# Kernel tuning notes

Measured on AMD Instinct MI355X. Metric: run time of the kernel, lower is better.

The kernel has to match this reference:

```python
import jax, jax.numpy as jnp
import numpy as np


def setup_inputs() -> dict:
    key = jax.random.key(0)
    ks = jax.random.split(key, 8)
    B, T, D = 4, 4096, 1024
    d_inner, dt_rank, d_state = 2048, 64, 16
    s = 0.02  # weight init scale for numerical stability
    f32 = jnp.float32
    return {
        "x": jax.random.normal(ks[0], (B, T, D), f32),
        "in_proj_w": jax.random.normal(ks[1], (2 * d_inner, D), f32) * s,
        "conv_w": jax.random.normal(ks[2], (d_inner, 1, 3), f32) * s,
        "conv_b": jnp.zeros((d_inner,), f32),
        "x_proj_w": jax.random.normal(ks[3], (dt_rank + 2 * d_state, d_inner), f32) * s,
        "dt_proj_w": jax.random.normal(ks[4], (d_inner, dt_rank), f32) * s,
        "dt_proj_b": jnp.zeros((d_inner,), f32),
        "D_param": jnp.ones((d_inner,), f32),
        "out_proj_w": jax.random.normal(ks[5], (D, d_inner), f32) * s,
    }


def reference(x, in_proj_w, conv_w, conv_b, x_proj_w, dt_proj_w, dt_proj_b, D_param, out_proj_w):
    d_inner = conv_b.shape[0]
    dt_rank = dt_proj_w.shape[1]

    # in_proj and split into x-branch / gate-branch z
    xz = jnp.einsum('btd,ed->bte', x, in_proj_w)          # [B,T,2*d_inner]
    xs, z = jnp.split(xz, 2, axis=-1)                     # each [B,T,d_inner]

    # depthwise conv1d along time (kernel 3, padding 1, groups=d_inner)
    xc = jnp.transpose(xs, (0, 2, 1))                     # [B,C,T]
    xc = jax.lax.conv_general_dilated(
        xc, conv_w, window_strides=(1,), padding=[(1, 1)],
        dimension_numbers=('NCH', 'OIH', 'NCH'), feature_group_count=d_inner)
    xc = xc + conv_b[None, :, None]
    xs = jnp.transpose(xc, (0, 2, 1))                     # [B,T,d_inner]

    # x_proj -> take dt part (B,C slices are unused by the scan math)
    x_dbl = jnp.einsum('btc,ec->bte', xs, x_proj_w)       # [B,T,dt_rank+2*d_state]
    dt = jnp.einsum('btr,cr->btc', x_dbl[..., :dt_rank], dt_proj_w) + dt_proj_b  # [B,T,d_inner]

    # selective scan: scalar gate per (batch, t); h_t = g*h_{t-1} + (1-g)*x_t
    gate = jax.nn.sigmoid(jnp.mean(dt, axis=-1))          # [B,T]

    def step(h, inp):
        g, xt = inp                                       # g: [B], xt: [B,d_inner]
        h_new = g[:, None] * h + (1.0 - g[:, None]) * xt
        return h_new, h_new

    h0 = jnp.zeros_like(xs[:, 0])                         # [B,d_inner]
    _, ys = jax.lax.scan(step, h0, (gate.T, jnp.transpose(xs, (1, 0, 2))))
    y = jnp.transpose(ys, (1, 0, 2))                      # [B,T,d_inner]

    y = y * jax.nn.silu(z) + D_param * xs
    return jnp.einsum('btc,dc->btd', y, out_proj_w)       # [B,T,d_model]
```

## Files before the change

### kernel.cpp

```cpp
#include <hip/hip_runtime.h>
#include <hip/hip_bf16.h>
#include <math.h>

#define B_ 4
#define T_ 4096
#define DM 1024
#define DI 2048
#define E2 4096
#define NCHUNK 128
#define CLEN 32

typedef __attribute__((ext_vector_type(8))) short short8;
typedef __attribute__((ext_vector_type(4))) float floatx4;

union bfs { __hip_bfloat16 b; short s; };

__device__ __forceinline__ float bf2f(__hip_bfloat16 x) { return __bfloat162float(x); }
__device__ __forceinline__ short f2s(float x) { bfs u; u.b = __float2bfloat16(x); return u.s; }

__device__ __forceinline__ float ldw(const void* p, int i, int f32m) {
    return f32m ? ((const float*)p)[i] : bf2f(((const __hip_bfloat16*)p)[i]);
}

#define GLDS16(gp, lp) __builtin_amdgcn_global_load_lds( \
    (const __attribute__((address_space(1))) void*)(gp), \
    (__attribute__((address_space(3))) void*)(lp), 16, 0, 0)

#define MEMFENCE asm volatile("" ::: "memory")

__global__ __launch_bounds__(256)
void detect_k(const unsigned short* __restrict__ xu, unsigned* __restrict__ flag)
{
    __shared__ int red[256];
    const int tid = threadIdx.x;
    int cnt = 0;
    for (int i = tid; i < 2048; i += 256) {
        const int e = (xu[i] >> 7) & 0xFF;
        cnt += (e >= 0x90);
    }
    red[tid] = cnt;
    __syncthreads();
    for (int off = 128; off; off >>= 1) {
        if (tid < off) red[tid] += red[tid + off];
        __syncthreads();
    }
    if (tid == 0) *flag = (red[0] >= 8) ? 1u : 0u;
}

__global__ __launch_bounds__(256)
void cvt_k(const void* __restrict__ src, __hip_bfloat16* __restrict__ dst,
           const unsigned* __restrict__ flag)
{
    const int fm = (int)*flag;
    const size_t i0 = ((size_t)blockIdx.x * 256 + threadIdx.x) * 8;
    if (fm) {
        const float* f = (const float*)src + i0;
        floatx4 lo = *(const floatx4*)f;
        floatx4 hi = *(const floatx4*)(f + 4);
        short8 r;
        r[0] = f2s(lo[0]); r[1] = f2s(lo[1]); r[2] = f2s(lo[2]); r[3] = f2s(lo[3]);
        r[4] = f2s(hi[0]); r[5] = f2s(hi[1]); r[6] = f2s(hi[2]); r[7] = f2s(hi[3]);
        *(short8*)(dst + i0) = r;
    } else {
        *(short8*)(dst + i0) = *(const short8*)((const __hip_bfloat16*)src + i0);
    }
}

__global__ __launch_bounds__(256)
void cvt_strided_k(const void* __restrict__ src, __hip_bfloat16* __restrict__ dst,
                   const unsigned* __restrict__ flag)
{
    const int fm = (int)*flag;
    const size_t i0 = ((size_t)blockIdx.x * 256 + threadIdx.x) * 8;
    const size_t row = i0 >> 11, col = i0 & 2047;
    __hip_bfloat16* d = dst + row * E2 + col;
    if (fm) {
        const float* f = (const float*)src + i0;
        floatx4 lo = *(const floatx4*)f;
        floatx4 hi = *(const floatx4*)(f + 4);
        short8 r;
        r[0] = f2s(lo[0]); r[1] = f2s(lo[1]); r[2] = f2s(lo[2]); r[3] = f2s(lo[3]);
        r[4] = f2s(hi[0]); r[5] = f2s(hi[1]); r[6] = f2s(hi[2]); r[7] = f2s(hi[3]);
        *(short8*)d = r;
    } else {
        *(short8*)d = *(const short8*)((const __hip_bfloat16*)src + i0);
    }
}

__global__ __launch_bounds__(512)
void gemm256(const __hip_bfloat16* __restrict__ A,
             const __hip_bfloat16* __restrict__ Bt,
             void* __restrict__ C, int K, int lda, int ldb, int ldc,
             int csel, const unsigned* __restrict__ flag)
{
    __shared__ __align__(16) char sL[4 * 32768];

    const int cf = csel & (int)*flag;

    const int tid  = threadIdx.x;
    const int lane = tid & 63;
    const int wid  = tid >> 6;
    const int wr   = wid >> 2;
    const int wc   = wid & 3;
    const int l15  = lane & 15;
    const int quad = lane >> 4;
    const int swl  = (l15 >> 1) & 3;

    const int m0 = blockIdx.x * 256;
    const int n0 = blockIdx.y * 256;

    floatx4 acc[8][4];
#pragma unroll
    for (int i = 0; i < 8; i++)
#pragma unroll
        for (int j = 0; j < 4; j++) acc[i][j] = (floatx4){0.f, 0.f, 0.f, 0.f};

    const int srow = tid >> 2;
    const int ksrc = (((tid & 3) ^ ((tid >> 3) & 3))) * 8;
    const __hip_bfloat16* gA = A  + (size_t)(m0 + srow) * lda + ksrc;
    const __hip_bfloat16* gB = Bt + (size_t)(n0 + srow) * ldb + ksrc;
    const size_t h1A = (size_t)128 * lda;
    const size_t h1B = (size_t)128 * ldb;

    char* const ldsW = sL + wid * 1024;

    const int NT = K >> 5;

#define STAGE_A(buf, kt) do { \
    const __hip_bfloat16* g_ = gA + (size_t)(kt) * 32; \
    char* l_ = ldsW + (buf) * 32768; \
    GLDS16(g_, l_); \
    GLDS16(g_ + h1A, l_ + 8192); } while (0)
#define STAGE_B(buf, kt) do { \
    const __hip_bfloat16* g_ = gB + (size_t)(kt) * 32; \
    char* l_ = ldsW + (buf) * 32768 + 16384; \
    GLDS16(g_, l_); \
    GLDS16(g_ + h1B, l_ + 8192); } while (0)

    STAGE_A(0, 0); STAGE_B(0, 0);
    STAGE_A(1, 1); STAGE_B(1, 1);
    STAGE_A(2, 2); STAGE_B(2, 2);
    asm volatile("s_waitcnt vmcnt(8)" ::: "memory");
    __builtin_amdgcn_s_barrier();
    MEMFENCE;

    for (int t = 0; t < NT; ++t) {
        const char* Ab = sL + (t & 3) * 32768;
        const char* Bb = Ab + 16384;
        const int nx = (t + 3) & 3;

        short8 fb[4], fa[4];
#pragma unroll
        for (int j = 0; j < 4; j++)
            fb[j] = *(const short8*)(Bb + (wc * 64 + j * 16 + l15) * 64 + ((quad ^ swl) * 16));
#pragma unroll
        for (int i = 0; i < 4; i++)
            fa[i] = *(const short8*)(Ab + (wr * 128 + i * 16 + l15) * 64 + ((quad ^ swl) * 16));
        if (t + 3 < NT) STAGE_A(nx, t + 3);
        __builtin_amdgcn_s_barrier();
        MEMFENCE;
        __builtin_amdgcn_s_setprio(1);
#pragma unroll
        for (int i = 0; i < 4; i++)
#pragma unroll
            for (int j = 0; j < 4; j++)
                acc[i][j] = __builtin_amdgcn_mfma_f32_16x16x32_bf16(fa[i], fb[j], acc[i][j], 0, 0, 0);
        __builtin_amdgcn_s_setprio(0);
        __builtin_amdgcn_s_barrier();
        MEMFENCE;

        short8 fa2[4];
#pragma unroll
        for (int i = 0; i < 4; i++)
            fa2[i] = *(const short8*)(Ab + (wr * 128 + 64 + i * 16 + l15) * 64 + ((quad ^ swl) * 16));
        if (t + 3 < NT) {
            STAGE_B(nx, t + 3);
            asm volatile("s_waitcnt vmcnt(8)" ::: "memory");
        } else {
            asm volatile("s_waitcnt vmcnt(0)" ::: "memory");
        }
        __builtin_amdgcn_s_barrier();
        MEMFENCE;
        __builtin_amdgcn_s_setprio(1);
#pragma unroll
        for (int i = 0; i < 4; i++)
#pragma unroll
            for (int j = 0; j < 4; j++)
                acc[4 + i][j] = __builtin_amdgcn_mfma_f32_16x16x32_bf16(fa2[i], fb[j], acc[4 + i][j], 0, 0, 0);
        __builtin_amdgcn_s_setprio(0);
        __builtin_amdgcn_s_barrier();
        MEMFENCE;
    }
#undef STAGE_A
#undef STAGE_B

#pragma unroll
    for (int i = 0; i < 8; i++) {
        const int row = m0 + wr * 128 + i * 16 + quad * 4;
#pragma unroll
        for (int j = 0; j < 4; j++) {
            const int col = n0 + wc * 64 + j * 16 + l15;
#pragma unroll
            for (int r = 0; r < 4; r++) {
                const size_t idx = (size_t)(row + r) * ldc + col;
                const float val = acc[i][j][r];
                if (cf) ((float*)C)[idx] = val;
                else    ((__hip_bfloat16*)C)[idx] = __float2bfloat16(val);
            }
        }
    }
}

__global__ __launch_bounds__(256)
void precompute_wm_k(const void* __restrict__ dtw, const void* __restrict__ dtb,
                     float* __restrict__ wm, const unsigned* __restrict__ flag)
{
    __shared__ float red[256];
    const int fm = (int)*flag;
    const int tid = threadIdx.x;
    const int r = blockIdx.x;
    float s = 0.f;
    if (r < 64) {
        for (int c = tid; c < DI; c += 256) s += ldw(dtw, c * 64 + r, fm);
    } else {
        for (int c = tid; c < DI; c += 256) s += ldw(dtb, c, fm);
    }
    red[tid] = s;
    __syncthreads();
    for (int off = 128; off; off >>= 1) {
        if (tid < off) red[tid] += red[tid + off];
        __syncthreads();
    }
    if (tid == 0) wm[r] = red[0] / (float)DI;
}

__global__ __launch_bounds__(256)
void precompute_v2_k(const void* __restrict__ xpw, const float* __restrict__ wm,
                     float* __restrict__ v, const unsigned* __restrict__ flag)
{
    const int fm = (int)*flag;
    const int c = blockIdx.x * 256 + threadIdx.x;
    float s = 0.f;
#pragma unroll
    for (int r = 0; r < 64; r++) s += wm[r] * ldw(xpw, r * DI + c, fm);
    v[c] = s;
    if (c == 0) v[DI] = wm[64];
}

__global__ __launch_bounds__(256)
void conv_gate_nox(const __hip_bfloat16* __restrict__ xz,
                   const void* __restrict__ cw, const void* __restrict__ cb,
                   const float* __restrict__ v, float* __restrict__ gate,
                   const unsigned* __restrict__ flag)
{
    __shared__ float red[256];
    const int fm = (int)*flag;
    const int t = blockIdx.x, b = blockIdx.y, tid = threadIdx.x;
    const size_t bt = (size_t)b * T_ + t;
    const __hip_bfloat16* row0 = xz + bt * E2;
    float partial = 0.f;
#pragma unroll
    for (int j = 0; j < 8; j++) {
        const int c = tid + j * 256;
        const float w0 = ldw(cw, c * 3 + 0, fm);
        const float w1 = ldw(cw, c * 3 + 1, fm);
        const float w2 = ldw(cw, c * 3 + 2, fm);
        const float xm = (t > 0)      ? bf2f(row0[(int)c - E2]) : 0.f;
        const float x0 = bf2f(row0[c]);
        const float xp = (t < T_ - 1) ? bf2f(row0[c + E2]) : 0.f;
        const float val = w0 * xm + w1 * x0 + w2 * xp + ldw(cb, c, fm);
        partial += v[c] * val;
    }
    red[tid] = partial;
    __syncthreads();
    for (int off = 128; off; off >>= 1) {
        if (tid < off) red[tid] += red[tid + off];
        __syncthreads();
    }
    if (tid == 0) {
        const float s = red[0] + v[DI];
        gate[bt] = 1.f / (1.f + __expf(-s));
    }
}

__global__ __launch_bounds__(256)
void pprod_k(const float* __restrict__ gate, float* __restrict__ P)
{
    const int gid = blockIdx.x * 256 + threadIdx.x;
    const int b = gid >> 7, ch = gid & 127;
    const float* g = gate + (size_t)b * T_ + ch * CLEN;
    float p = 1.f;
#pragma unroll
    for (int i = 0; i < CLEN; i++) p *= g[i];
    P[gid] = p;
}

__global__ __launch_bounds__(256)
void scan_chunks(const __hip_bfloat16* __restrict__ xz,
                 const float* __restrict__ gate,
                 const void* __restrict__ cw, const void* __restrict__ cb,
                 float* __restrict__ r, const unsigned* __restrict__ flag)
{
    const int fm = (int)*flag;
    const int blk = blockIdx.x;
    const int cg = blk & 7, chunk = (blk >> 3) & 127, b = blk >> 10;
    const int c = cg * 256 + threadIdx.x;
    const float w0 = ldw(cw, c * 3 + 0, fm);
    const float w1 = ldw(cw, c * 3 + 1, fm);
    const float w2 = ldw(cw, c * 3 + 2, fm);
    const float bc = ldw(cb, c, fm);
    const int t0 = chunk * CLEN;
    const float* g = gate + (size_t)b * T_ + t0;
    const __hip_bfloat16* px = xz + (size_t)b * T_ * E2 + c;

    float xm = (t0 > 0) ? bf2f(px[(size_t)(t0 - 1) * E2]) : 0.f;
    float xc = bf2f(px[(size_t)t0 * E2]);
    float h = 0.f;
#pragma unroll 4
    for (int i = 0; i < CLEN; i++) {
        const int t = t0 + i;
        const float xn = (t + 1 < T_) ? bf2f(px[(size_t)(t + 1) * E2]) : 0.f;
        const float val = w0 * xm + w1 * xc + w2 * xn + bc;
        const float gi = g[i];
        h = gi * h + (1.f - gi) * val;
        xm = xc; xc = xn;
    }
    r[((size_t)b * NCHUNK + chunk) * DI + c] = h;
}

__global__ __launch_bounds__(256)
void carry_fix(float* __restrict__ r, const float* __restrict__ P)
{
    const int gid = blockIdx.x * 256 + threadIdx.x;
    const int b = gid >> 11, c = gid & 2047;
    float h = 0.f;
    for (int k = 0; k < NCHUNK; k++) {
        const size_t idx = ((size_t)b * NCHUNK + k) * DI + c;
        const float rk = r[idx];
        const float Pk = P[b * NCHUNK + k];
        r[idx] = h;
        h = Pk * h + rk;
    }
}

__global__ __launch_bounds__(256)
void scan_apply(__hip_bfloat16* __restrict__ xz,
                const float* __restrict__ gate,
                const float* __restrict__ r,
                const void* __restrict__ cw, const void* __restrict__ cb,
                const void* __restrict__ Dp, const unsigned* __restrict__ flag)
{
    const int fm = (int)*flag;
    const int blk = blockIdx.x;
    const int cg = blk & 7, chunk = (blk >> 3) & 127, b = blk >> 10;
    const int c = cg * 256 + threadIdx.x;
    const float w0 = ldw(cw, c * 3 + 0, fm);
    const float w1 = ldw(cw, c * 3 + 1, fm);
    const float w2 = ldw(cw, c * 3 + 2, fm);
    const float bc = ldw(cb, c, fm);
    const float Dc = ldw(Dp, c, fm);
    const int t0 = chunk * CLEN;
    const float* g = gate + (size_t)b * T_ + t0;
    const __hip_bfloat16* px = xz + (size_t)b * T_ * E2 + c;
    __hip_bfloat16* pz = xz + (size_t)b * T_ * E2 + DI + c;

    float h = r[((size_t)b * NCHUNK + chunk) * DI + c];
    float xm = (t0 > 0) ? bf2f(px[(size_t)(t0 - 1) * E2]) : 0.f;
    float xc = bf2f(px[(size_t)t0 * E2]);
#pragma unroll 4
    for (int i = 0; i < CLEN; i++) {
        const int t = t0 + i;
        const float xn = (t + 1 < T_) ? bf2f(px[(size_t)(t + 1) * E2]) : 0.f;
        const float val = w0 * xm + w1 * xc + w2 * xn + bc;
        const float gi = g[i];
        h = gi * h + (1.f - gi) * val;
        const float zv = bf2f(pz[(size_t)t * E2]);
        const float sil = zv / (1.f + __expf(-zv));
        pz[(size_t)t * E2] = __float2bfloat16(h * sil + Dc * val);
        xm = xc; xc = xn;
    }
}

extern "C" void kernel_launch(void* const* d_in, const int* in_sizes, int n_in,
                              void* d_out, int out_size, void* d_ws, size_t ws_size,
                              hipStream_t stream)
{
    const size_t REQUIRED = 134292480;
    if (ws_size < REQUIRED) return;

    const void* x    = d_in[0];
    const void* wip  = d_in[1];
    const void* cw   = d_in[2];
    const void* cb   = d_in[3];
    const void* xpw  = d_in[4];
    const void* dtw  = d_in[5];
    const void* dtb  = d_in[6];
    const void* Dp   = d_in[7];
    const void* wop  = d_in[8];

    char* ws = (char*)d_ws;
    __hip_bfloat16* xz = (__hip_bfloat16*)ws;
    float* gate    = (float*)(ws + 134217728);
    float* v       = (float*)(ws + 134283264);
    float* wm      = v + 2052;
    unsigned* flag = (unsigned*)(ws + 134291968);

    __hip_bfloat16* x_bf   = (__hip_bfloat16*)d_out;
    __hip_bfloat16* wip_bf = (__hip_bfloat16*)((char*)d_out + 33554432);
    float* r = (float*)((char*)d_out + 41943040);
    float* P = (float*)((char*)d_out + 46137344);
    __hip_bfloat16* wop_bf = xz;

    detect_k<<<1, 256, 0, stream>>>((const unsigned short*)x, flag);

    cvt_k<<<8192, 256, 0, stream>>>(x, x_bf, flag);
    cvt_k<<<2048, 256, 0, stream>>>(wip, wip_bf, flag);

    precompute_wm_k<<<65, 256, 0, stream>>>(dtw, dtb, wm, flag);
    precompute_v2_k<<<8, 256, 0, stream>>>(xpw, wm, v, flag);

    gemm256<<<dim3(64, 16), 512, 0, stream>>>(x_bf, wip_bf, xz,
                                              1024, 1024, 1024, E2, 0, flag);

    conv_gate_nox<<<dim3(T_, B_), 256, 0, stream>>>(xz, cw, cb, v, gate, flag);

    pprod_k<<<2, 256, 0, stream>>>(gate, P);
    scan_chunks<<<4096, 256, 0, stream>>>(xz, gate, cw, cb, r, flag);
    carry_fix<<<32, 256, 0, stream>>>(r, P);
    scan_apply<<<4096, 256, 0, stream>>>(xz, gate, r, cw, cb, Dp, flag);

    cvt_strided_k<<<1024, 256, 0, stream>>>(wop, wop_bf, flag);

    gemm256<<<dim3(64, 4), 512, 0, stream>>>(xz + DI, wop_bf, d_out,
                                             2048, E2, E2, DM, 1, flag);
}
```

Measured before the change: 516.3 us.

## Factor conv out of gate dot product and double scan chunk length

The gate logit is rewritten algebraically: the depthwise conv weights are folded into three per-channel vectors, so each timestep reads its own xs row once and computes three dot products. Neighbouring timesteps' partial sums are then combined in a small finishing kernel, replacing the three-row-per-timestep reads of the old conv_gate kernel. The scan chunk count is also halved to 64 chunks of 64 steps, which halves the number of scan blocks and carry entries but lengthens the serial work in each thread. The change adds extra kernel launches and scratch buffers for the partial sums.

New measurement: 455.0 us. 11.9% less time.

```diff
diff --git a/kernel.cpp b/kernel.cpp
--- a/kernel.cpp
+++ b/kernel.cpp
@@ -7,8 +7,8 @@
 #define DM 1024
 #define DI 2048
 #define E2 4096
-#define NCHUNK 128
-#define CLEN 32
+#define NCHUNK 64
+#define CLEN 64
 
 typedef __attribute__((ext_vector_type(8))) short short8;
 typedef __attribute__((ext_vector_type(4))) float floatx4;
@@ -236,63 +236,108 @@
 
 __global__ __launch_bounds__(256)
 void precompute_v2_k(const void* __restrict__ xpw, const float* __restrict__ wm,
-                     float* __restrict__ v, const unsigned* __restrict__ flag)
-{
-    const int fm = (int)*flag;
-    const int c = blockIdx.x * 256 + threadIdx.x;
+                     const void* __restrict__ cw, const void* __restrict__ cb,
+                     float* __restrict__ v,
+                     float* __restrict__ u0, float* __restrict__ u1,
+                     float* __restrict__ u2, float* __restrict__ gcpart,
+                     const unsigned* __restrict__ flag)
+{
+    __shared__ float red[256];
+    const int fm = (int)*flag;
+    const int tid = threadIdx.x;
+    const int c = blockIdx.x * 256 + tid;
     float s = 0.f;
 #pragma unroll
     for (int r = 0; r < 64; r++) s += wm[r] * ldw(xpw, r * DI + c, fm);
     v[c] = s;
+    u0[c] = s * ldw(cw, c * 3 + 0, fm);
+    u1[c] = s * ldw(cw, c * 3 + 1, fm);
+    u2[c] = s * ldw(cw, c * 3 + 2, fm);
     if (c == 0) v[DI] = wm[64];
-}
-
-__global__ __launch_bounds__(256)
-void conv_gate_nox(const __hip_bfloat16* __restrict__ xz,
-                   const void* __restrict__ cw, const void* __restrict__ cb,
-                   const float* __restrict__ v, float* __restrict__ gate,
-                   const unsigned* __restrict__ flag)
-{
-    __shared__ float red[256];
-    const int fm = (int)*flag;
-    const int t = blockIdx.x, b = blockIdx.y, tid = threadIdx.x;
-    const size_t bt = (size_t)b * T_ + t;
-    const __hip_bfloat16* row0 = xz + bt * E2;
-    float partial = 0.f;
-#pragma unroll
-    for (int j = 0; j < 8; j++) {
-        const int c = tid + j * 256;
-        const float w0 = ldw(cw, c * 3 + 0, fm);
-        const float w1 = ldw(cw, c * 3 + 1, fm);
-        const float w2 = ldw(cw, c * 3 + 2, fm);
-        const float xm = (t > 0)      ? bf2f(row0[(int)c - E2]) : 0.f;
-        const float x0 = bf2f(row0[c]);
-        const float xp = (t < T_ - 1) ? bf2f(row0[c + E2]) : 0.f;
-        const float val = w0 * xm + w1 * x0 + w2 * xp + ldw(cb, c, fm);
-        partial += v[c] * val;
-    }
-    red[tid] = partial;
+
+    red[tid] = s * ldw(cb, c, fm);
     __syncthreads();
     for (int off = 128; off; off >>= 1) {
         if (tid < off) red[tid] += red[tid + off];
         __syncthreads();
     }
-    if (tid == 0) {
-        const float s = red[0] + v[DI];
-        gate[bt] = 1.f / (1.f + __expf(-s));
-    }
+    if (tid == 0) gcpart[blockIdx.x] = red[0];
+}
+
+__global__ __launch_bounds__(256)
+void gate_dots_k(const __hip_bfloat16* __restrict__ xz,
+                 const float* __restrict__ u0, const float* __restrict__ u1,
+                 const float* __restrict__ u2,
+                 float* __restrict__ S0, float* __restrict__ S1,
+                 float* __restrict__ S2)
+{
+    __shared__ float red[12];
+    const int t = blockIdx.x, b = blockIdx.y, tid = threadIdx.x;
+    const size_t bt = (size_t)b * T_ + t;
+    const int c0 = tid * 8;
+    const short8 xv = *(const short8*)(xz + bt * E2 + c0);
+    const floatx4 a0 = *(const floatx4*)(u0 + c0);
+    const floatx4 b0 = *(const floatx4*)(u0 + c0 + 4);
+    const floatx4 a1 = *(const floatx4*)(u1 + c0);
+    const floatx4 b1 = *(const floatx4*)(u1 + c0 + 4);
+    const floatx4 a2 = *(const floatx4*)(u2 + c0);
+    const floatx4 b2 = *(const floatx4*)(u2 + c0 + 4);
+    float s0 = 0.f, s1 = 0.f, s2 = 0.f;
+#pragma unroll
+    for (int j = 0; j < 4; j++) {
+        bfs w; w.s = xv[j];
+        const float xf = bf2f(w.b);
+        s0 += a0[j] * xf; s1 += a1[j] * xf; s2 += a2[j] * xf;
+    }
+#pragma unroll
+    for (int j = 0; j < 4; j++) {
+        bfs w; w.s = xv[4 + j];
+        const float xf = bf2f(w.b);
+        s0 += b0[j] * xf; s1 += b1[j] * xf; s2 += b2[j] * xf;
+    }
+#pragma unroll
+    for (int off = 32; off; off >>= 1) {
+        s0 += __shfl_xor(s0, off);
+        s1 += __shfl_xor(s1, off);
+        s2 += __shfl_xor(s2, off);
+    }
+    const int wv = tid >> 6;
+    if ((tid & 63) == 0) { red[wv * 3] = s0; red[wv * 3 + 1] = s1; red[wv * 3 + 2] = s2; }
+    __syncthreads();
+    if (tid < 3) {
+        const float r = red[tid] + red[3 + tid] + red[6 + tid] + red[9 + tid];
+        if (tid == 0) S0[bt] = r;
+        else if (tid == 1) S1[bt] = r;
+        else S2[bt] = r;
+    }
+}
+
+__global__ __launch_bounds__(256)
+void gate_fin_k(const float* __restrict__ S0, const float* __restrict__ S1,
+                const float* __restrict__ S2, const float* __restrict__ gcpart,
+                const float* __restrict__ v, float* __restrict__ gate)
+{
+    const int gid = blockIdx.x * 256 + threadIdx.x;
+    const int t = gid & (T_ - 1);
+    float k = v[DI];
+#pragma unroll
+    for (int i = 0; i < 8; i++) k += gcpart[i];
+    float lg = S1[gid] + k;
+    if (t > 0)      lg += S0[gid - 1];
+    if (t < T_ - 1) lg += S2[gid + 1];
+    gate[gid] = 1.f / (1.f + __expf(-lg));
 }
 
 __global__ __launch_bounds__(256)
 void pprod_k(const float* __restrict__ gate, float* __restrict__ P)
 {
-    const int gid = blockIdx.x * 256 + threadIdx.x;
-    const int b = gid >> 7, ch = gid & 127;
+    const int tid = threadIdx.x;
+    const int b = tid >> 6, ch = tid & 63;
     const float* g = gate + (size_t)b * T_ + ch * CLEN;
     float p = 1.f;
 #pragma unroll
     for (int i = 0; i < CLEN; i++) p *= g[i];
-    P[gid] = p;
+    P[tid] = p;
 }
 
 __global__ __launch_bounds__(256)
@@ -303,7 +348,7 @@
 {
     const int fm = (int)*flag;
     const int blk = blockIdx.x;
-    const int cg = blk & 7, chunk = (blk >> 3) & 127, b = blk >> 10;
+    const int cg = blk & 7, chunk = (blk >> 3) & 63, b = blk >> 9;
     const int c = cg * 256 + threadIdx.x;
     const float w0 = ldw(cw, c * 3 + 0, fm);
     const float w1 = ldw(cw, c * 3 + 1, fm);
@@ -352,7 +397,7 @@
 {
     const int fm = (int)*flag;
     const int blk = blockIdx.x;
-    const int cg = blk & 7, chunk = (blk >> 3) & 127, b = blk >> 10;
+    const int cg = blk & 7, chunk = (blk >> 3) & 63, b = blk >> 9;
     const int c = cg * 256 + threadIdx.x;
     const float w0 = ldw(cw, c * 3 + 0, fm);
     const float w1 = ldw(cw, c * 3 + 1, fm);
@@ -407,8 +452,15 @@
 
     __hip_bfloat16* x_bf   = (__hip_bfloat16*)d_out;
     __hip_bfloat16* wip_bf = (__hip_bfloat16*)((char*)d_out + 33554432);
-    float* r = (float*)((char*)d_out + 41943040);
-    float* P = (float*)((char*)d_out + 46137344);
+    float* r      = (float*)((char*)d_out + 41943040);
+    float* P      = (float*)((char*)d_out + 44040192);
+    float* u0     = (float*)((char*)d_out + 44041216);
+    float* u1     = (float*)((char*)d_out + 44049408);
+    float* u2     = (float*)((char*)d_out + 44057600);
+    float* gcpart = (float*)((char*)d_out + 44065792);
+    float* S0     = (float*)((char*)d_out + 44065824);
+    float* S1     = (float*)((char*)d_out + 44131360);
+    float* S2     = (float*)((char*)d_out + 44196896);
     __hip_bfloat16* wop_bf = xz;
 
     detect_k<<<1, 256, 0, stream>>>((const unsigned short*)x, flag);
@@ -417,17 +469,19 @@
     cvt_k<<<2048, 256, 0, stream>>>(wip, wip_bf, flag);
 
     precompute_wm_k<<<65, 256, 0, stream>>>(dtw, dtb, wm, flag);
-    precompute_v2_k<<<8, 256, 0, stream>>>(xpw, wm, v, flag);
+    precompute_v2_k<<<8, 256, 0, stream>>>(xpw, wm, cw, cb, v, u0, u1, u2,
+                                           gcpart, flag);
 
     gemm256<<<dim3(64, 16), 512, 0, stream>>>(x_bf, wip_bf, xz,
                                               1024, 1024, 1024, E2, 0, flag);
 
-    conv_gate_nox<<<dim3(T_, B_), 256, 0, stream>>>(xz, cw, cb, v, gate, flag);
-
-    pprod_k<<<2, 256, 0, stream>>>(gate, P);
-    scan_chunks<<<4096, 256, 0, stream>>>(xz, gate, cw, cb, r, flag);
+    gate_dots_k<<<dim3(T_, B_), 256, 0, stream>>>(xz, u0, u1, u2, S0, S1, S2);
+    gate_fin_k<<<64, 256, 0, stream>>>(S0, S1, S2, gcpart, v, gate);
+
+    pprod_k<<<1, 256, 0, stream>>>(gate, P);
+    scan_chunks<<<2048, 256, 0, stream>>>(xz, gate, cw, cb, r, flag);
     carry_fix<<<32, 256, 0, stream>>>(r, P);
-    scan_apply<<<4096, 256, 0, stream>>>(xz, gate, r, cw, cb, Dp, flag);
+    scan_apply<<<2048, 256, 0, stream>>>(xz, gate, r, cw, cb, Dp, flag);
 
     cvt_strided_k<<<1024, 256, 0, stream>>>(wop, wop_bf, flag);
 
```

## Fuse conv, gate reduction, chunk scan and product into one kernel

Applied to the files above, without the earlier changes.

Replaces the separate conv_gate, pprod and scan_chunks kernels with one fused kernel. Each block computes the conv output, the per-timestep gate reduction and the chunk-local scan over a 64-step chunk, so the xs rows are read once instead of twice. The apply kernel is vectorised to 4 channels per thread with register prefetch of x and z rows. Chunks grow to 64 steps, and the grids shrink sharply (256 blocks of 512 threads, 512 blocks of 256). That risks low occupancy, and the fused kernel adds two block barriers per timestep.

After: 481.1 us. 6.8% less time.

```diff
diff --git a/kernel.cpp b/kernel.cpp
--- a/kernel.cpp
+++ b/kernel.cpp
@@ -7,10 +7,11 @@
 #define DM 1024
 #define DI 2048
 #define E2 4096
-#define NCHUNK 128
-#define CLEN 32
+#define NCHUNK 64
+#define CLEN 64
 
 typedef __attribute__((ext_vector_type(8))) short short8;
+typedef __attribute__((ext_vector_type(4))) short short4v;
 typedef __attribute__((ext_vector_type(4))) float floatx4;
 
 union bfs { __hip_bfloat16 b; short s; };
@@ -247,85 +248,83 @@
     if (c == 0) v[DI] = wm[64];
 }
 
-__global__ __launch_bounds__(256)
-void conv_gate_nox(const __hip_bfloat16* __restrict__ xz,
-                   const void* __restrict__ cw, const void* __restrict__ cb,
-                   const float* __restrict__ v, float* __restrict__ gate,
-                   const unsigned* __restrict__ flag)
-{
-    __shared__ float red[256];
-    const int fm = (int)*flag;
-    const int t = blockIdx.x, b = blockIdx.y, tid = threadIdx.x;
-    const size_t bt = (size_t)b * T_ + t;
-    const __hip_bfloat16* row0 = xz + bt * E2;
-    float partial = 0.f;
-#pragma unroll
-    for (int j = 0; j < 8; j++) {
-        const int c = tid + j * 256;
-        const float w0 = ldw(cw, c * 3 + 0, fm);
-        const float w1 = ldw(cw, c * 3 + 1, fm);
-        const float w2 = ldw(cw, c * 3 + 2, fm);
-        const float xm = (t > 0)      ? bf2f(row0[(int)c - E2]) : 0.f;
-        const float x0 = bf2f(row0[c]);
-        const float xp = (t < T_ - 1) ? bf2f(row0[c + E2]) : 0.f;
-        const float val = w0 * xm + w1 * x0 + w2 * xp + ldw(cb, c, fm);
-        partial += v[c] * val;
-    }
-    red[tid] = partial;
-    __syncthreads();
-    for (int off = 128; off; off >>= 1) {
-        if (tid < off) red[tid] += red[tid + off];
-        __syncthreads();
-    }
-    if (tid == 0) {
-        const float s = red[0] + v[DI];
-        gate[bt] = 1.f / (1.f + __expf(-s));
-    }
-}
-
-__global__ __launch_bounds__(256)
-void pprod_k(const float* __restrict__ gate, float* __restrict__ P)
-{
-    const int gid = blockIdx.x * 256 + threadIdx.x;
-    const int b = gid >> 7, ch = gid & 127;
-    const float* g = gate + (size_t)b * T_ + ch * CLEN;
+#define LOADROW(dst, tt) do { \
+    if ((tt) >= 0 && (tt) < T_) { \
+        short4v _x = *(const short4v*)(px + (size_t)(tt) * E2); \
+        bfs _u; \
+        _u.s = _x[0]; dst[0] = bf2f(_u.b); \
+        _u.s = _x[1]; dst[1] = bf2f(_u.b); \
+        _u.s = _x[2]; dst[2] = bf2f(_u.b); \
+        _u.s = _x[3]; dst[3] = bf2f(_u.b); \
+    } else { dst[0] = dst[1] = dst[2] = dst[3] = 0.f; } \
+} while (0)
+
+__global__ __launch_bounds__(512)
+void fused_scan1(const __hip_bfloat16* __restrict__ xz,
+                 const void* __restrict__ cw, const void* __restrict__ cb,
+                 const float* __restrict__ v,
+                 float* __restrict__ r, float* __restrict__ gate,
+                 float* __restrict__ P, const unsigned* __restrict__ flag)
+{
+    __shared__ float red[8];
+    const int fm = (int)*flag;
+    const int chunk = blockIdx.x, b = blockIdx.y;
+    const int tid = threadIdx.x;
+    const int c0 = tid * 4;
+
+    float w0[4], w1[4], w2[4], bcv[4], vc[4];
+#pragma unroll
+    for (int k = 0; k < 4; k++) {
+        const int c = c0 + k;
+        w0[k]  = ldw(cw, c * 3 + 0, fm);
+        w1[k]  = ldw(cw, c * 3 + 1, fm);
+        w2[k]  = ldw(cw, c * 3 + 2, fm);
+        bcv[k] = ldw(cb, c, fm);
+        vc[k]  = v[c];
+    }
+    const float vb = v[DI];
+    const int t0 = chunk * CLEN;
+    const __hip_bfloat16* px = xz + (size_t)b * T_ * E2 + c0;
+
+    float x0[4], x1[4], x2[4], x3[4];
+    LOADROW(x0, t0 - 1);
+    LOADROW(x1, t0);
+    LOADROW(x2, t0 + 1);
+    LOADROW(x3, t0 + 2);
+
+    float h[4] = {0.f, 0.f, 0.f, 0.f};
     float p = 1.f;
-#pragma unroll
-    for (int i = 0; i < CLEN; i++) p *= g[i];
-    P[gid] = p;
-}
-
-__global__ __launch_bounds__(256)
-void scan_chunks(const __hip_bfloat16* __restrict__ xz,
-                 const float* __restrict__ gate,
-                 const void* __restrict__ cw, const void* __restrict__ cb,
-                 float* __restrict__ r, const unsigned* __restrict__ flag)
-{
-    const int fm = (int)*flag;
-    const int blk = blockIdx.x;
-    const int cg = blk & 7, chunk = (blk >> 3) & 127, b = blk >> 10;
-    const int c = cg * 256 + threadIdx.x;
-    const float w0 = ldw(cw, c * 3 + 0, fm);
-    const float w1 = ldw(cw, c * 3 + 1, fm);
-    const float w2 = ldw(cw, c * 3 + 2, fm);
-    const float bc = ldw(cb, c, fm);
-    const int t0 = chunk * CLEN;
-    const float* g = gate + (size_t)b * T_ + t0;
-    const __hip_bfloat16* px = xz + (size_t)b * T_ * E2 + c;
-
-    float xm = (t0 > 0) ? bf2f(px[(size_t)(t0 - 1) * E2]) : 0.f;
-    float xc = bf2f(px[(size_t)t0 * E2]);
-    float h = 0.f;
 #pragma unroll 4
     for (int i = 0; i < CLEN; i++) {
         const int t = t0 + i;
-        const float xn = (t + 1 < T_) ? bf2f(px[(size_t)(t + 1) * E2]) : 0.f;
-        const float val = w0 * xm + w1 * xc + w2 * xn + bc;
-        const float gi = g[i];
-        h = gi * h + (1.f - gi) * val;
-        xm = xc; xc = xn;
-    }
-    r[((size_t)b * NCHUNK + chunk) * DI + c] = h;
+        float xf[4];
+        LOADROW(xf, t + 3);
+        float val[4];
+        float part = 0.f;
+#pragma unroll
+        for (int k = 0; k < 4; k++) {
+            val[k] = w0[k] * x0[k] + w1[k] * x1[k] + w2[k] * x2[k] + bcv[k];
+            part += vc[k] * val[k];
+        }
+#pragma unroll
+        for (int off = 32; off; off >>= 1) part += __shfl_xor(part, off);
+        if ((tid & 63) == 0) red[tid >> 6] = part;
+        __syncthreads();
+        float lg = vb;
+#pragma unroll
+        for (int wvi = 0; wvi < 8; wvi++) lg += red[wvi];
+        __syncthreads();
+        const float g = 1.f / (1.f + __expf(-lg));
+#pragma unroll
+        for (int k = 0; k < 4; k++) h[k] = g * h[k] + (1.f - g) * val[k];
+        p *= g;
+        if (tid == 0) gate[(size_t)b * T_ + t] = g;
+#pragma unroll
+        for (int k = 0; k < 4; k++) { x0[k] = x1[k]; x1[k] = x2[k]; x2[k] = x3[k]; x3[k] = xf[k]; }
+    }
+    *(floatx4*)(r + ((size_t)b * NCHUNK + chunk) * DI + c0) =
+        (floatx4){h[0], h[1], h[2], h[3]};
+    if (tid == 0) P[b * NCHUNK + chunk] = p;
 }
 
 __global__ __launch_bounds__(256)
@@ -344,41 +343,81 @@
 }
 
 __global__ __launch_bounds__(256)
-void scan_apply(__hip_bfloat16* __restrict__ xz,
-                const float* __restrict__ gate,
-                const float* __restrict__ r,
-                const void* __restrict__ cw, const void* __restrict__ cb,
-                const void* __restrict__ Dp, const unsigned* __restrict__ flag)
+void scan_apply2(__hip_bfloat16* __restrict__ xz,
+                 const float* __restrict__ gate, const float* __restrict__ r,
+                 const void* __restrict__ cw, const void* __restrict__ cb,
+                 const void* __restrict__ Dp, const unsigned* __restrict__ flag)
 {
     const int fm = (int)*flag;
     const int blk = blockIdx.x;
-    const int cg = blk & 7, chunk = (blk >> 3) & 127, b = blk >> 10;
-    const int c = cg * 256 + threadIdx.x;
-    const float w0 = ldw(cw, c * 3 + 0, fm);
-    const float w1 = ldw(cw, c * 3 + 1, fm);
-    const float w2 = ldw(cw, c * 3 + 2, fm);
-    const float bc = ldw(cb, c, fm);
-    const float Dc = ldw(Dp, c, fm);
+    const int half = blk & 1, chunk = (blk >> 1) & 63, b = blk >> 7;
+    const int c0 = half * 1024 + threadIdx.x * 4;
+
+    float w0[4], w1[4], w2[4], bcv[4], Dc[4];
+#pragma unroll
+    for (int k = 0; k < 4; k++) {
+        const int c = c0 + k;
+        w0[k]  = ldw(cw, c * 3 + 0, fm);
+        w1[k]  = ldw(cw, c * 3 + 1, fm);
+        w2[k]  = ldw(cw, c * 3 + 2, fm);
+        bcv[k] = ldw(cb, c, fm);
+        Dc[k]  = ldw(Dp, c, fm);
+    }
     const int t0 = chunk * CLEN;
     const float* g = gate + (size_t)b * T_ + t0;
-    const __hip_bfloat16* px = xz + (size_t)b * T_ * E2 + c;
-    __hip_bfloat16* pz = xz + (size_t)b * T_ * E2 + DI + c;
-
-    float h = r[((size_t)b * NCHUNK + chunk) * DI + c];
-    float xm = (t0 > 0) ? bf2f(px[(size_t)(t0 - 1) * E2]) : 0.f;
-    float xc = bf2f(px[(size_t)t0 * E2]);
+    const __hip_bfloat16* px = xz + (size_t)b * T_ * E2 + c0;
+    __hip_bfloat16* pz = xz + (size_t)b * T_ * E2 + DI + c0;
+
+    float h[4];
+    {
+        floatx4 hv = *(const floatx4*)(r + ((size_t)b * NCHUNK + chunk) * DI + c0);
+        h[0] = hv[0]; h[1] = hv[1]; h[2] = hv[2]; h[3] = hv[3];
+    }
+
+    float x0[4], x1[4], x2[4], x3[4];
+    LOADROW(x0, t0 - 1);
+    LOADROW(x1, t0);
+    LOADROW(x2, t0 + 1);
+    LOADROW(x3, t0 + 2);
+
+    float z0[4], z1[4], z2[4];
+#define LOADZ(dst, tt) do { \
+    if ((tt) < T_) { \
+        short4v _z = *(const short4v*)(pz + (size_t)(tt) * E2); \
+        bfs _u; \
+        _u.s = _z[0]; dst[0] = bf2f(_u.b); \
+        _u.s = _z[1]; dst[1] = bf2f(_u.b); \
+        _u.s = _z[2]; dst[2] = bf2f(_u.b); \
+        _u.s = _z[3]; dst[3] = bf2f(_u.b); \
+    } else { dst[0] = dst[1] = dst[2] = dst[3] = 0.f; } \
+} while (0)
+    LOADZ(z0, t0);
+    LOADZ(z1, t0 + 1);
+    LOADZ(z2, t0 + 2);
+
 #pragma unroll 4
     for (int i = 0; i < CLEN; i++) {
         const int t = t0 + i;
-        const float xn = (t + 1 < T_) ? bf2f(px[(size_t)(t + 1) * E2]) : 0.f;
-        const float val = w0 * xm + w1 * xc + w2 * xn + bc;
+        float xf[4], zf[4];
+        LOADROW(xf, t + 3);
+        LOADZ(zf, t + 3);
         const float gi = g[i];
-        h = gi * h + (1.f - gi) * val;
-        const float zv = bf2f(pz[(size_t)t * E2]);
-        const float sil = zv / (1.f + __expf(-zv));
-        pz[(size_t)t * E2] = __float2bfloat16(h * sil + Dc * val);
-        xm = xc; xc = xn;
-    }
+        short4v yv;
+#pragma unroll
+        for (int k = 0; k < 4; k++) {
+            const float val = w0[k] * x0[k] + w1[k] * x1[k] + w2[k] * x2[k] + bcv[k];
+            h[k] = gi * h[k] + (1.f - gi) * val;
+            const float sil = z0[k] / (1.f + __expf(-z0[k]));
+            yv[k] = f2s(h[k] * sil + Dc[k] * val);
+        }
+        *(short4v*)(pz + (size_t)t * E2) = yv;
+#pragma unroll
+        for (int k = 0; k < 4; k++) {
+            x0[k] = x1[k]; x1[k] = x2[k]; x2[k] = x3[k]; x3[k] = xf[k];
+            z0[k] = z1[k]; z1[k] = z2[k]; z2[k] = zf[k];
+        }
+    }
+#undef LOADZ
 }
 
 extern "C" void kernel_launch(void* const* d_in, const int* in_sizes, int n_in,
@@ -408,7 +447,7 @@
     __hip_bfloat16* x_bf   = (__hip_bfloat16*)d_out;
     __hip_bfloat16* wip_bf = (__hip_bfloat16*)((char*)d_out + 33554432);
     float* r = (float*)((char*)d_out + 41943040);
-    float* P = (float*)((char*)d_out + 46137344);
+    float* P = (float*)((char*)d_out + 44040192);
     __hip_bfloat16* wop_bf = xz;
 
     detect_k<<<1, 256, 0, stream>>>((const unsigned short*)x, flag);
@@ -422,12 +461,10 @@
     gemm256<<<dim3(64, 16), 512, 0, stream>>>(x_bf, wip_bf, xz,
                                               1024, 1024, 1024, E2, 0, flag);
 
-    conv_gate_nox<<<dim3(T_, B_), 256, 0, stream>>>(xz, cw, cb, v, gate, flag);
-
-    pprod_k<<<2, 256, 0, stream>>>(gate, P);
-    scan_chunks<<<4096, 256, 0, stream>>>(xz, gate, cw, cb, r, flag);
+    fused_scan1<<<dim3(NCHUNK, B_), 512, 0, stream>>>(xz, cw, cb, v,
+                                                      r, gate, P, flag);
     carry_fix<<<32, 256, 0, stream>>>(r, P);
-    scan_apply<<<4096, 256, 0, stream>>>(xz, gate, r, cw, cb, Dp, flag);
+    scan_apply2<<<512, 256, 0, stream>>>(xz, gate, r, cw, cb, Dp, flag);
 
     cvt_strided_k<<<1024, 256, 0, stream>>>(wop, wop_bf, flag);
 
```
